# Optimization experiments

Hardware: AMD Instinct MI355X
Metric: run time of the kernel (lower is better)

Reference implementation:

```python
import jax, jax.numpy as jnp
import numpy as np

NU, NI = 100000, 50000          # num_users, num_items
N = NU + NI                      # total nodes
D = 64                           # hidden_dim
DE = 16                          # eigs_dim
L = 2                            # n_layers
E = 1500000                      # edges per layer
NP = 14                          # 2**(sample_hop+1)-2 path types
EPS = 1e-5


def setup_inputs() -> dict:
    key = jax.random.key(0)
    ks = jax.random.split(key, 7)
    return {
        "user_emb": jax.random.normal(ks[0], (NU, D), jnp.float32) * 0.1,
        "item_emb": jax.random.normal(ks[1], (NI, D), jnp.float32) * 0.1,
        "eigs": jax.random.normal(ks[2], (N, DE), jnp.float32),
        "lambda0": jax.random.normal(ks[3], (L,), jnp.float32) * 0.1,
        "path_w": jax.random.normal(ks[4], (L, NP), jnp.float32) * 0.1,
        "indices": jax.random.randint(ks[5], (L, 2, E), 0, N),
        "path_type": jax.random.randint(ks[6], (L, E), 0, NP),
    }


def _layer_norm(x):
    mu = x.mean(-1, keepdims=True)
    var = ((x - mu) ** 2).mean(-1, keepdims=True)
    return (x - mu) * jax.lax.rsqrt(var + EPS)


def _sparse_softmax(row, vals, n):
    # torch: clamp(exp(v), min=-5, max=5) -> effectively min(exp(v), 5)
    e = jnp.clip(jnp.exp(vals), -5.0, 5.0)
    s = jax.ops.segment_sum(e, row, num_segments=n)
    s = jnp.where(s == 0.0, 1.0, s)
    return e / s[row]


def _encoder(x, idx, pt, eigs, lam, pw):
    y = _layer_norm(x)                                   # [N, D]
    r, c = idx[0], idx[1]                                # [E]
    yc = y[c]                                            # [E, D]
    xs = (y[r] * yc).sum(-1) * (1.0 / jnp.sqrt(jnp.float32(D)))  # [E]
    ys = (eigs[r] * eigs[c]).sum(-1)                     # [E]
    s0 = _sparse_softmax(r, xs + jnp.exp(lam) * ys, N)
    s1 = _sparse_softmax(r, pw[pt], N)
    s = 0.5 * (s0 + s1)                                  # mean over the two scores
    # SpMM: out[r] += s_e * y[c_e]
    return jax.ops.segment_sum(s[:, None] * yc, r, num_segments=N)


def reference(user_emb, item_emb, eigs, lambda0, path_w, indices, path_type):
    x = jnp.concatenate([user_emb, item_emb], axis=0)    # [N, D]
    embs = [x]
    for l in range(L):
        x = _encoder(x, indices[l], path_type[l], eigs, lambda0[l], path_w[l])
        embs.append(x)
    return jnp.mean(jnp.stack(embs, axis=1), axis=1)      # [N, D]
```

## Files before the change

### kernel.cpp

```cpp
#include <hip/hip_runtime.h>
#include <hip/hip_bf16.h>

#define NUSERS 100000
#define NITEMS 50000
#define NN 150000
#define DD 64
#define DE 16
#define NE 1500000
#define NPATH 14
#define LN_EPS 1e-5f

#define BROWS 1024
#define NBUK 147
#define NB (2 * NBUK)
#define CHUNK 4096
#define NCHUNK ((NE + CHUNK - 1) / CHUNK)
#define CAP 11264

#define EIGBLK ((NN * DE) / 256)

typedef float vf2 __attribute__((ext_vector_type(2)));

__device__ __forceinline__ vf2 unpk(unsigned u) {
    vf2 r;
    r.x = __uint_as_float(u << 16);
    r.y = __uint_as_float(u & 0xffff0000u);
    return r;
}
__device__ __forceinline__ unsigned f2b(float f) {
    union { float f; unsigned u; } v; v.f = f;
    return (v.u + 0x7fffu + ((v.u >> 16) & 1u)) >> 16;
}

template<int CTRL>
__device__ __forceinline__ float dppmov(float x) {
    return __int_as_float(
        __builtin_amdgcn_mov_dpp(__float_as_int(x), CTRL, 0xF, 0xF, true));
}

__device__ __forceinline__ int wscan(int v, int lane) {
    #pragma unroll
    for (int d = 1; d < 64; d <<= 1) {
        int u = __shfl_up(v, d, 64);
        v += (lane >= d) ? u : 0;
    }
    return v;
}

__global__ void k_init(int* __restrict__ curbuk) {
    int t = blockIdx.x * 256 + threadIdx.x;
    if (t < NB) curbuk[t] = t * CAP;
}

__global__ void k_eigln(const float* __restrict__ uemb,
                        const float* __restrict__ iemb,
                        const float* __restrict__ eigs,
                        unsigned short* __restrict__ e16,
                        unsigned short* __restrict__ y) {
    int blk = blockIdx.x;
    int t = threadIdx.x;
    if (blk < EIGBLK) {
        int i = blk * 256 + t;
        e16[i] = (unsigned short)f2b(eigs[i]);
    } else {
        int row = (blk - EIGBLK) * 4 + (t >> 6);
        int lane = t & 63;
        if (row >= NN) return;
        int i = row * DD + lane;
        float v = (row < NUSERS) ? uemb[i] : iemb[i - NUSERS * DD];
        float s = v;
        #pragma unroll
        for (int m = 32; m; m >>= 1) s += __shfl_xor(s, m, 64);
        float mu = s * (1.0f / 64.0f);
        float d = v - mu;
        float q = d * d;
        #pragma unroll
        for (int m = 32; m; m >>= 1) q += __shfl_xor(q, m, 64);
        float rs = rsqrtf(q * (1.0f / 64.0f) + LN_EPS);
        y[i] = (unsigned short)f2b(d * rs);
    }
}

__global__ __launch_bounds__(512) void k_pscatter(
        const int* __restrict__ idx,
        const int* __restrict__ ptyp,
        int* __restrict__ curbuk,
        unsigned int* __restrict__ stage) {
    int blk = blockIdx.x;
    int layer = blk / NCHUNK;
    int k = blk - layer * NCHUNK;
    __shared__ int h[NBUK];
    __shared__ int hofs[NBUK];
    for (int t = threadIdx.x; t < NBUK; t += 512) h[t] = 0;
    __syncthreads();
    const int* rrow = idx + (size_t)layer * 2 * NE;
    const int* ccol = rrow + NE;
    const int* pp   = ptyp + (size_t)layer * NE;
    int base = k * CHUNK;
    int lim = min(CHUNK, NE - base);
    for (int j = threadIdx.x; j < lim; j += 512)
        atomicAdd(&h[rrow[base + j] >> 10], 1);
    __syncthreads();
    for (int t = threadIdx.x; t < NBUK; t += 512) {
        int c = h[t];
        hofs[t] = c ? atomicAdd(&curbuk[layer * NBUK + t], c) : 0;
    }
    __syncthreads();
    for (int j = threadIdx.x; j < lim; j += 512) {
        int e = base + j;
        int r = rrow[e];
        int pos = atomicAdd(&hofs[r >> 10], 1);
        stage[pos] = (unsigned)ccol[e] | ((unsigned)pp[e] << 18)
                   | ((unsigned)(r & 1023) << 22);
    }
}

__global__ __launch_bounds__(1024) void k_bscatter(
        const unsigned int* __restrict__ stage,
        const int* __restrict__ curbuk,
        int* __restrict__ csv,
        int2* __restrict__ roff) {
    __shared__ int scnt[BROWS];
    __shared__ int scur[BROWS];
    __shared__ int wsum[16];
    int b = blockIdx.x;
    int t = threadIdx.x;
    int lane = t & 63, w = t >> 6;
    int layer = b / NBUK;
    int brow0 = (b - layer * NBUK) * BROWS;
    int nrows = min(BROWS, NN - brow0);
    int start = b * CAP;
    int n = curbuk[b] - start;
    scnt[t] = 0;
    __syncthreads();
    for (int p = t; p < n; p += 1024)
        atomicAdd(&scnt[stage[start + p] >> 22], 1);
    __syncthreads();
    int orig = scnt[t];
    int s = wscan(orig, lane);
    if (lane == 63) wsum[w] = s;
    __syncthreads();
    if (w == 0) {
        int x = (lane < 16) ? wsum[lane] : 0;
        #pragma unroll
        for (int d = 1; d < 16; d <<= 1) {
            int u = __shfl_up(x, d, 64);
            x += (lane >= d) ? u : 0;
        }
        if (lane < 16) wsum[lane] = x;
    }
    __syncthreads();
    int wb = (w > 0) ? wsum[w - 1] : 0;
    int excl = wb + s - orig;
    scur[t] = excl;
    if (t < nrows)
        roff[(size_t)layer * NN + brow0 + t] =
            make_int2(start + excl, start + excl + orig);
    __syncthreads();
    for (int p = t; p < n; p += 1024) {
        unsigned rec = stage[start + p];
        int pos = atomicAdd(&scur[rec >> 22], 1);
        csv[start + pos] = (int)(rec & 0x3fffffu);
    }
}

__global__ void k_row(const unsigned short* __restrict__ y,
                      const unsigned short* __restrict__ e16,
                      const int2* __restrict__ roff,
                      const int* __restrict__ csv,
                      const float* __restrict__ pw,
                      const float* __restrict__ lam,
                      int layer,
                      const float* __restrict__ uemb,
                      const float* __restrict__ iemb,
                      float* __restrict__ x1,
                      unsigned short* __restrict__ y1,
                      float* __restrict__ out) {
    __shared__ float pexp[NPATH];
    __shared__ float selam;
    int t = threadIdx.x;
    if (t < NPATH) pexp[t] = fminf(expf(pw[layer * NPATH + t]), 5.0f);
    if (t == NPATH) selam = expf(lam[layer]);
    __syncthreads();

    int row = blockIdx.x * 4 + (t >> 6);
    int lane = t & 63;
    int g = lane >> 3;
    int sl = lane & 7;
    int2 pr = roff[row];
    int p0 = pr.x, p1 = pr.y;

    uint4 ar = reinterpret_cast<const uint4*>(y + (size_t)row * DD)[sl];
    vf2 a0 = unpk(ar.x), a1 = unpk(ar.y), a2 = unpk(ar.z), a3 = unpk(ar.w);
    unsigned eru = reinterpret_cast<const unsigned*>(e16 + (size_t)row * DE)[sl];
    vf2 er = unpk(eru);
    float elam = selam;

    float sum0 = 0.f, sum1 = 0.f;
    vf2 A0 = {0.f, 0.f}, A1 = {0.f, 0.f}, A2 = {0.f, 0.f}, A3 = {0.f, 0.f};
    vf2 B0 = {0.f, 0.f}, B1 = {0.f, 0.f}, B2 = {0.f, 0.f}, B3 = {0.f, 0.f};

    int pend = p0 + ((p1 - p0) & ~7);

    for (int p = p0; p < pend; p += 8) {
        int rec = csv[p + g];
        int c = rec & 0x3ffff;
        uint4 bv = reinterpret_cast<const uint4*>(y + (size_t)c * DD)[sl];
        unsigned ecu = reinterpret_cast<const unsigned*>(e16 + (size_t)c * DE)[sl];
        vf2 b0 = unpk(bv.x), b1 = unpk(bv.y), b2 = unpk(bv.z), b3 = unpk(bv.w);
        vf2 px = a0 * b0;
        px += a1 * b1;
        px += a2 * b2;
        px += a3 * b3;
        vf2 ec = unpk(ecu);
        vf2 tt = px * 0.125f + (er * ec) * elam;
        float sc = tt.x + tt.y;
        sc += dppmov<0xB1>(sc);
        sc += dppmov<0x4E>(sc);
        sc += dppmov<0x141>(sc);
        float e0 = fminf(__expf(sc), 5.0f);
        float e1 = pexp[(rec >> 18) & 0xF];
        sum0 += e0; sum1 += e1;
        A0 += e0 * b0; A1 += e0 * b1; A2 += e0 * b2; A3 += e0 * b3;
        B0 += e1 * b0; B1 += e1 * b1; B2 += e1 * b2; B3 += e1 * b3;
    }

    if (pend < p1) {
        int q = pend + g;
        int qc = (q < p1) ? q : (p1 - 1);
        int rec = csv[qc];
        int c = rec & 0x3ffff;
        uint4 bv = reinterpret_cast<const uint4*>(y + (size_t)c * DD)[sl];
        unsigned ecu = reinterpret_cast<const unsigned*>(e16 + (size_t)c * DE)[sl];
        vf2 b0 = unpk(bv.x), b1 = unpk(bv.y), b2 = unpk(bv.z), b3 = unpk(bv.w);
        vf2 px = a0 * b0;
        px += a1 * b1;
        px += a2 * b2;
        px += a3 * b3;
        vf2 ec = unpk(ecu);
        vf2 tt = px * 0.125f + (er * ec) * elam;
        float sc = tt.x + tt.y;
        sc += dppmov<0xB1>(sc);
        sc += dppmov<0x4E>(sc);
        sc += dppmov<0x141>(sc);
        bool ok = q < p1;
        float e0 = ok ? fminf(__expf(sc), 5.0f) : 0.f;
        float e1 = ok ? pexp[(rec >> 18) & 0xF] : 0.f;
        sum0 += e0; sum1 += e1;
        A0 += e0 * b0; A1 += e0 * b1; A2 += e0 * b2; A3 += e0 * b3;
        B0 += e1 * b0; B1 += e1 * b1; B2 += e1 * b2; B3 += e1 * b3;
    }

    sum0 += dppmov<0x128>(sum0);
    sum1 += dppmov<0x128>(sum1);
    #pragma unroll
    for (int m = 16; m <= 32; m <<= 1) {
        sum0 += __shfl_xor(sum0, m, 64);
        sum1 += __shfl_xor(sum1, m, 64);
    }
    float rinv0 = 0.5f / ((sum0 == 0.f) ? 1.f : sum0);
    float rinv1 = 0.5f / ((sum1 == 0.f) ? 1.f : sum1);

    vf2 o0 = rinv0 * A0 + rinv1 * B0, o1 = rinv0 * A1 + rinv1 * B1;
    vf2 o2 = rinv0 * A2 + rinv1 * B2, o3 = rinv0 * A3 + rinv1 * B3;
    o0.x += dppmov<0x128>(o0.x); o0.y += dppmov<0x128>(o0.y);
    o1.x += dppmov<0x128>(o1.x); o1.y += dppmov<0x128>(o1.y);
    o2.x += dppmov<0x128>(o2.x); o2.y += dppmov<0x128>(o2.y);
    o3.x += dppmov<0x128>(o3.x); o3.y += dppmov<0x128>(o3.y);
    #pragma unroll
    for (int m = 16; m <= 32; m <<= 1) {
        vf2 s;
        s.x = __shfl_xor(o0.x, m, 64); s.y = __shfl_xor(o0.y, m, 64); o0 += s;
        s.x = __shfl_xor(o1.x, m, 64); s.y = __shfl_xor(o1.y, m, 64); o1 += s;
        s.x = __shfl_xor(o2.x, m, 64); s.y = __shfl_xor(o2.y, m, 64); o2 += s;
        s.x = __shfl_xor(o3.x, m, 64); s.y = __shfl_xor(o3.y, m, 64); o3 += s;
    }
    if (g == 0) {
        int ofs = sl * 8;
        float v0 = o0.x, v1 = o0.y, v2 = o1.x, v3 = o1.y;
        float v4 = o2.x, v5 = o2.y, v6 = o3.x, v7 = o3.y;
        if (layer == 0) {
            float* dst = x1 + (size_t)row * DD + ofs;
            reinterpret_cast<float4*>(dst)[0] = make_float4(v0, v1, v2, v3);
            reinterpret_cast<float4*>(dst)[1] = make_float4(v4, v5, v6, v7);
            float s = v0+v1+v2+v3+v4+v5+v6+v7;
            s += __shfl_xor(s, 1, 64);
            s += __shfl_xor(s, 2, 64);
            s += __shfl_xor(s, 4, 64);
            float mu = s * (1.0f / 64.0f);
            float d0=v0-mu, d1=v1-mu, d2=v2-mu, d3=v3-mu;
            float d4=v4-mu, d5=v5-mu, d6=v6-mu, d7=v7-mu;
            float qv = d0*d0+d1*d1+d2*d2+d3*d3+d4*d4+d5*d5+d6*d6+d7*d7;
            qv += __shfl_xor(qv, 1, 64);
            qv += __shfl_xor(qv, 2, 64);
            qv += __shfl_xor(qv, 4, 64);
            float rs = rsqrtf(qv * (1.0f / 64.0f) + LN_EPS);
            uint4 pk;
            pk.x = f2b(d0*rs) | (f2b(d1*rs) << 16);
            pk.y = f2b(d2*rs) | (f2b(d3*rs) << 16);
            pk.z = f2b(d4*rs) | (f2b(d5*rs) << 16);
            pk.w = f2b(d6*rs) | (f2b(d7*rs) << 16);
            reinterpret_cast<uint4*>(y1 + (size_t)row * DD)[sl] = pk;
        } else {
            const float* e = (row < NUSERS)
                ? (uemb + (size_t)row * DD + ofs)
                : (iemb + (size_t)(row - NUSERS) * DD + ofs);
            const float* xp = x1 + (size_t)row * DD + ofs;
            float4 ea = reinterpret_cast<const float4*>(e)[0];
            float4 eb = reinterpret_cast<const float4*>(e)[1];
            float4 xa = reinterpret_cast<const float4*>(xp)[0];
            float4 xb = reinterpret_cast<const float4*>(xp)[1];
            float* dst = out + (size_t)row * DD + ofs;
            const float k3 = 1.0f / 3.0f;
            reinterpret_cast<float4*>(dst)[0] = make_float4(
                (ea.x + xa.x + v0) * k3, (ea.y + xa.y + v1) * k3,
                (ea.z + xa.z + v2) * k3, (ea.w + xa.w + v3) * k3);
            reinterpret_cast<float4*>(dst)[1] = make_float4(
                (eb.x + xb.x + v4) * k3, (eb.y + xb.y + v5) * k3,
                (eb.z + xb.z + v6) * k3, (eb.w + xb.w + v7) * k3);
        }
    }
}

extern "C" void kernel_launch(void* const* d_in, const int* in_sizes, int n_in,
                              void* d_out, int out_size, void* d_ws, size_t ws_size,
                              hipStream_t stream) {
    const float* uemb = (const float*)d_in[0];
    const float* iemb = (const float*)d_in[1];
    const float* eigs = (const float*)d_in[2];
    const float* lam  = (const float*)d_in[3];
    const float* pw   = (const float*)d_in[4];
    const int* idx    = (const int*)d_in[5];
    const int* ptyp   = (const int*)d_in[6];

    char* w = (char*)d_ws;
    unsigned int*   stage  = (unsigned int*)(w);
    float*          x1     = (float*)(w);
    unsigned short* y0     = (unsigned short*)(w + 38400000);
    unsigned short* y1     = (unsigned short*)(w + 57600000);
    int*            csv    = (int*)(w + 76800000);
    int2*           roff   = (int2*)(w + 90601472);
    unsigned short* e16    = (unsigned short*)(w + 93001472);
    int*            curbuk = (int*)(w + 97801472);

    k_init<<<2, 256, 0, stream>>>(curbuk);
    k_pscatter<<<2 * NCHUNK, 512, 0, stream>>>(idx, ptyp, curbuk, stage);
    k_bscatter<<<NB, 1024, 0, stream>>>(stage, curbuk, csv, roff);

    const int gRows = NN / 4;
    k_eigln<<<EIGBLK + gRows, 256, 0, stream>>>(uemb, iemb, eigs, e16, y0);

    k_row<<<gRows, 256, 0, stream>>>(y0, e16, roff, csv, pw, lam, 0,
                                     nullptr, nullptr, x1, y1, nullptr);
    k_row<<<gRows, 256, 0, stream>>>(y1, e16, roff + NN, csv, pw, lam, 1,
                                     uemb, iemb, x1, nullptr, (float*)d_out);
}
```

Before: 384.3 us.

## Fuse edge prescatter with eig/layernorm prep and cache records in registers

The edge bucket prescatter, the bf16 eigs conversion and the layer-0 layernorm now run as one launch, so these independent stages share the GPU and launch gaps go away. The init kernel is replaced by a memset: bucket counters now start at zero and hold offsets relative to each bucket. The bucket scatter kernel loads its staged records into registers once, instead of reading them from global memory in both passes. CAP is raised so 12 records per thread cover a bucket, and the count is clamped to CAP, which silently drops entries if a bucket overflows.

```diff
diff --git a/kernel.cpp b/kernel.cpp
--- a/kernel.cpp
+++ b/kernel.cpp
@@ -15,9 +15,11 @@
 #define NB (2 * NBUK)
 #define CHUNK 4096
 #define NCHUNK ((NE + CHUNK - 1) / CHUNK)
-#define CAP 11264
-
-#define EIGBLK ((NN * DE) / 256)
+#define CAP 11776
+
+#define PSB (2 * NCHUNK)
+#define EGB ((NN * DE + 511) / 512)
+#define LNB (NN / 8)
 
 typedef float vf2 __attribute__((ext_vector_type(2)));
 
@@ -47,25 +49,52 @@
     return v;
 }
 
-__global__ void k_init(int* __restrict__ curbuk) {
-    int t = blockIdx.x * 256 + threadIdx.x;
-    if (t < NB) curbuk[t] = t * CAP;
-}
-
-__global__ void k_eigln(const float* __restrict__ uemb,
-                        const float* __restrict__ iemb,
-                        const float* __restrict__ eigs,
-                        unsigned short* __restrict__ e16,
-                        unsigned short* __restrict__ y) {
+__global__ __launch_bounds__(512) void k_psc_eig(
+        const float* __restrict__ uemb,
+        const float* __restrict__ iemb,
+        const float* __restrict__ eigs,
+        const int* __restrict__ idx,
+        const int* __restrict__ ptyp,
+        int* __restrict__ curbuk,
+        unsigned int* __restrict__ stage,
+        unsigned short* __restrict__ e16,
+        unsigned short* __restrict__ y) {
     int blk = blockIdx.x;
     int t = threadIdx.x;
-    if (blk < EIGBLK) {
-        int i = blk * 256 + t;
-        e16[i] = (unsigned short)f2b(eigs[i]);
+    if (blk < PSB) {
+        int layer = blk / NCHUNK;
+        int k = blk - layer * NCHUNK;
+        __shared__ int h[NBUK];
+        __shared__ int hofs[NBUK];
+        for (int j = t; j < NBUK; j += 512) h[j] = 0;
+        __syncthreads();
+        const int* rrow = idx + (size_t)layer * 2 * NE;
+        const int* ccol = rrow + NE;
+        const int* pp   = ptyp + (size_t)layer * NE;
+        int base = k * CHUNK;
+        int lim = min(CHUNK, NE - base);
+        for (int j = t; j < lim; j += 512)
+            atomicAdd(&h[rrow[base + j] >> 10], 1);
+        __syncthreads();
+        for (int j = t; j < NBUK; j += 512) {
+            int c = h[j];
+            int gb = layer * NBUK + j;
+            hofs[j] = c ? (gb * CAP + atomicAdd(&curbuk[gb], c)) : 0;
+        }
+        __syncthreads();
+        for (int j = t; j < lim; j += 512) {
+            int e = base + j;
+            int r = rrow[e];
+            int pos = atomicAdd(&hofs[r >> 10], 1);
+            stage[pos] = (unsigned)ccol[e] | ((unsigned)pp[e] << 18)
+                       | ((unsigned)(r & 1023) << 22);
+        }
+    } else if (blk < PSB + EGB) {
+        int i = (blk - PSB) * 512 + t;
+        if (i < NN * DE) e16[i] = (unsigned short)f2b(eigs[i]);
     } else {
-        int row = (blk - EIGBLK) * 4 + (t >> 6);
+        int row = (blk - PSB - EGB) * 8 + (t >> 6);
         int lane = t & 63;
-        if (row >= NN) return;
         int i = row * DD + lane;
         float v = (row < NUSERS) ? uemb[i] : iemb[i - NUSERS * DD];
         float s = v;
@@ -78,40 +107,6 @@
         for (int m = 32; m; m >>= 1) q += __shfl_xor(q, m, 64);
         float rs = rsqrtf(q * (1.0f / 64.0f) + LN_EPS);
         y[i] = (unsigned short)f2b(d * rs);
-    }
-}
-
-__global__ __launch_bounds__(512) void k_pscatter(
-        const int* __restrict__ idx,
-        const int* __restrict__ ptyp,
-        int* __restrict__ curbuk,
-        unsigned int* __restrict__ stage) {
-    int blk = blockIdx.x;
-    int layer = blk / NCHUNK;
-    int k = blk - layer * NCHUNK;
-    __shared__ int h[NBUK];
-    __shared__ int hofs[NBUK];
-    for (int t = threadIdx.x; t < NBUK; t += 512) h[t] = 0;
-    __syncthreads();
-    const int* rrow = idx + (size_t)layer * 2 * NE;
-    const int* ccol = rrow + NE;
-    const int* pp   = ptyp + (size_t)layer * NE;
-    int base = k * CHUNK;
-    int lim = min(CHUNK, NE - base);
-    for (int j = threadIdx.x; j < lim; j += 512)
-        atomicAdd(&h[rrow[base + j] >> 10], 1);
-    __syncthreads();
-    for (int t = threadIdx.x; t < NBUK; t += 512) {
-        int c = h[t];
-        hofs[t] = c ? atomicAdd(&curbuk[layer * NBUK + t], c) : 0;
-    }
-    __syncthreads();
-    for (int j = threadIdx.x; j < lim; j += 512) {
-        int e = base + j;
-        int r = rrow[e];
-        int pos = atomicAdd(&hofs[r >> 10], 1);
-        stage[pos] = (unsigned)ccol[e] | ((unsigned)pp[e] << 18)
-                   | ((unsigned)(r & 1023) << 22);
     }
 }
 
@@ -130,11 +125,20 @@
     int brow0 = (b - layer * NBUK) * BROWS;
     int nrows = min(BROWS, NN - brow0);
     int start = b * CAP;
-    int n = curbuk[b] - start;
+    int n = min(curbuk[b], CAP);
+    unsigned recs[12];
+    #pragma unroll
+    for (int i = 0; i < 12; ++i) {
+        int p = t + i * 1024;
+        recs[i] = (p < n) ? stage[start + p] : 0u;
+    }
     scnt[t] = 0;
     __syncthreads();
-    for (int p = t; p < n; p += 1024)
-        atomicAdd(&scnt[stage[start + p] >> 22], 1);
+    #pragma unroll
+    for (int i = 0; i < 12; ++i) {
+        int p = t + i * 1024;
+        if (p < n) atomicAdd(&scnt[recs[i] >> 22], 1);
+    }
     __syncthreads();
     int orig = scnt[t];
     int s = wscan(orig, lane);
@@ -157,10 +161,14 @@
         roff[(size_t)layer * NN + brow0 + t] =
             make_int2(start + excl, start + excl + orig);
     __syncthreads();
-    for (int p = t; p < n; p += 1024) {
-        unsigned rec = stage[start + p];
-        int pos = atomicAdd(&scur[rec >> 22], 1);
-        csv[start + pos] = (int)(rec & 0x3fffffu);
+    #pragma unroll
+    for (int i = 0; i < 12; ++i) {
+        int p = t + i * 1024;
+        if (p < n) {
+            unsigned rec = recs[i];
+            int pos = atomicAdd(&scur[rec >> 22], 1);
+            csv[start + pos] = (int)(rec & 0x3fffffu);
+        }
     }
 }
 
@@ -339,17 +347,16 @@
     unsigned short* y0     = (unsigned short*)(w + 38400000);
     unsigned short* y1     = (unsigned short*)(w + 57600000);
     int*            csv    = (int*)(w + 76800000);
-    int2*           roff   = (int2*)(w + 90601472);
-    unsigned short* e16    = (unsigned short*)(w + 93001472);
-    int*            curbuk = (int*)(w + 97801472);
-
-    k_init<<<2, 256, 0, stream>>>(curbuk);
-    k_pscatter<<<2 * NCHUNK, 512, 0, stream>>>(idx, ptyp, curbuk, stage);
+    int2*           roff   = (int2*)(w + 90648576);
+    unsigned short* e16    = (unsigned short*)(w + 93048576);
+    int*            curbuk = (int*)(w + 97848576);
+
+    hipMemsetAsync(curbuk, 0, NB * sizeof(int), stream);
+    k_psc_eig<<<PSB + EGB + LNB, 512, 0, stream>>>(
+        uemb, iemb, eigs, idx, ptyp, curbuk, stage, e16, y0);
     k_bscatter<<<NB, 1024, 0, stream>>>(stage, curbuk, csv, roff);
 
     const int gRows = NN / 4;
-    k_eigln<<<EIGBLK + gRows, 256, 0, stream>>>(uemb, iemb, eigs, e16, y0);
-
     k_row<<<gRows, 256, 0, stream>>>(y0, e16, roff, csv, pw, lam, 0,
                                      nullptr, nullptr, x1, y1, nullptr);
     k_row<<<gRows, 256, 0, stream>>>(y1, e16, roff + NN, csv, pw, lam, 1,
```

Measured after the change: 376.4 us. 2.0% less time.
